# Kernel tuning notes

Hardware: AMD Instinct MI355X
Metric: run time of the kernel (lower is better)

## Reference

```python
import jax, jax.numpy as jnp
from jax import lax
import numpy as np

B, N, K, H = 8, 4096, 24, 32  # graphs, nodes/graph, kNN k, hidden_dim


def setup_inputs() -> dict:
    key = jax.random.key(0)
    ks = jax.random.split(key, 16)
    W = lambda k, i, o: jax.random.normal(k, (i, o), jnp.float32) * 0.1
    b = lambda k, o: jax.random.normal(k, (o,), jnp.float32) * 0.01
    inp = {
        'x_lc': jax.random.normal(ks[0], (B * N, 4), jnp.float32),
        'batch_lc': jnp.repeat(jnp.arange(B, dtype=jnp.int64), N),
        'enc_w1': W(ks[1], 4, H), 'enc_b1': b(ks[2], H),
        'enc_w2': W(ks[3], H, H), 'enc_b2': b(ks[4], H),
        'conv1_w': W(ks[5], 2 * H, H), 'conv1_b': b(ks[6], H),
        'conv2_w': W(ks[7], 2 * H, H), 'conv2_b': b(ks[8], H),
        'conv3_w': W(ks[9], 2 * H, H), 'conv3_b': b(ks[10], H),
        'out_w1': W(ks[11], H, 32), 'out_b1': b(ks[12], 32),
        'out_w2': W(ks[13], 32, 16), 'out_b2': b(ks[14], 16),
        'out_w3': W(ks[15], 16, 8), 'out_b3': jnp.zeros((8,), jnp.float32),
    }
    return inp


def _dynamic_edge_conv(x, w, bias):
    # x: [B, N, D]; kNN within each graph, edge msg nn([x_i, x_j - x_i]), max-agg
    d2 = jnp.sum(x * x, axis=-1)  # [B, N]
    dist = d2[:, :, None] + d2[:, None, :] - 2.0 * jnp.einsum('bnd,bmd->bnm', x, x)
    # kNN index computation is non-differentiable (as in PyG knn)
    idx = lax.top_k(-lax.stop_gradient(dist), K)[1]  # [B, N, K], includes self
    xj = jax.vmap(lambda xb, ib: xb[ib])(x, idx)  # [B, N, K, D]
    xi = jnp.broadcast_to(x[:, :, None, :], xj.shape)
    e = jnp.concatenate([xi, xj - xi], axis=-1)  # [B, N, K, 2D]
    h = jax.nn.elu(e @ w + bias)  # [B, N, K, H]
    return jnp.max(h, axis=2)  # [B, N, H]


def reference(x_lc, batch_lc, enc_w1, enc_b1, enc_w2, enc_b2,
              conv1_w, conv1_b, conv2_w, conv2_b, conv3_w, conv3_b,
              out_w1, out_b1, out_w2, out_b2, out_w3, out_b3):
    # lc_encode
    h = jax.nn.elu(x_lc @ enc_w1 + enc_b1)
    h = jax.nn.elu(h @ enc_w2 + enc_b2)  # [B*N, H]
    h = h.reshape(B, N, H)  # equal-sized sorted graphs
    h = _dynamic_edge_conv(h, conv1_w, conv1_b)
    h = _dynamic_edge_conv(h, conv2_w, conv2_b)
    h = _dynamic_edge_conv(h, conv3_w, conv3_b)
    h = h.reshape(B * N, H)
    o = jax.nn.elu(h @ out_w1 + out_b1)
    o = jax.nn.elu(o @ out_w2 + out_b2)
    o = o @ out_w3 + out_b3  # [B*N, 8]
    return (o, batch_lc)
```

## Files before the change

kernel.cpp:

```cpp
#include <hip/hip_runtime.h>
#include <cstddef>
#include <cstdint>

#define BN    32768
#define NG    4096
#define KNN   24
#define KPW   14
#define KM    32
#define CHK   128
#define NBQ   64
#define STKD  16
#define TRIG  13

typedef float f32x4_t __attribute__((ext_vector_type(4)));
typedef short s16x8_t __attribute__((ext_vector_type(8)));

__device__ __forceinline__ float elu_f(float x) {
    return x > 0.f ? x : expm1f(x);
}

__device__ __forceinline__ unsigned short f2bf(float f) {
    unsigned u = __float_as_uint(f);
    unsigned r = (u + 0x7FFFu + ((u >> 16) & 1u)) >> 16;
    return (unsigned short)r;
}

__device__ __forceinline__ void gload_lds16(const void* g, void* l) {
    __builtin_amdgcn_global_load_lds(
        (const __attribute__((address_space(1))) unsigned*)g,
        (__attribute__((address_space(3))) unsigned*)l, 16, 0, 0);
}

__device__ __forceinline__ void pack_node(int n, const float* hv,
    unsigned short* __restrict__ hbf, unsigned short* __restrict__ til,
    float* __restrict__ d2b)
{
    __align__(16) unsigned short us[32];
    float s = 0.f;
#pragma unroll
    for (int k = 0; k < 32; ++k) {
        us[k] = f2bf(hv[k]);
        float v = __uint_as_float(((unsigned)us[k]) << 16);
        s = fmaf(v, v, s);
    }
    d2b[n] = s;
    const uint4* up = reinterpret_cast<const uint4*>(us);
    uint4* lp = reinterpret_cast<uint4*>(hbf + (size_t)n * 32);
#pragma unroll
    for (int j = 0; j < 4; ++j) lp[j] = up[j];
    const int g = n >> 12, ln = n & 4095, tile = ln >> 4, c = ln & 15;
    unsigned short* tb = til + (size_t)g * 131072 + tile * 512 + c * 8;
#pragma unroll
    for (int kg = 0; kg < 4; ++kg)
        *reinterpret_cast<uint4*>(tb + kg * 128) = up[kg];
}

__global__ __launch_bounds__(128) void k_encoder(
    const float* __restrict__ x,
    const float* __restrict__ w1, const float* __restrict__ b1,
    const float* __restrict__ w2, const float* __restrict__ b2,
    float* __restrict__ hOut, float* __restrict__ d2Out,
    unsigned short* __restrict__ hbf, unsigned short* __restrict__ til,
    float* __restrict__ d2b)
{
    __shared__ float sw1[4 * 32];
    __shared__ float sb1[32];
    __shared__ float sw2[32 * 32];
    __shared__ float sb2[32];
    int tid = threadIdx.x;
    sw1[tid] = w1[tid];
    if (tid < 32) sb1[tid] = b1[tid];
    for (int i = tid; i < 1024; i += 128) sw2[i] = w2[i];
    if (tid >= 32 && tid < 64) sb2[tid - 32] = b2[tid - 32];
    __syncthreads();

    int node = blockIdx.x * 128 + tid;
    float4 xv = reinterpret_cast<const float4*>(x)[node];

    float h1[32];
#pragma unroll
    for (int o = 0; o < 32; ++o) {
        float s = sb1[o];
        s = fmaf(xv.x, sw1[o], s);
        s = fmaf(xv.y, sw1[32 + o], s);
        s = fmaf(xv.z, sw1[64 + o], s);
        s = fmaf(xv.w, sw1[96 + o], s);
        h1[o] = elu_f(s);
    }
    float h2[32];
    float d2 = 0.f;
#pragma unroll
    for (int o = 0; o < 32; ++o) {
        float s = sb2[o];
#pragma unroll
        for (int f = 0; f < 32; ++f) s = fmaf(h1[f], sw2[f * 32 + o], s);
        float v = elu_f(s);
        h2[o] = v;
        d2 = fmaf(v, v, d2);
    }
    float4* hp = reinterpret_cast<float4*>(hOut) + (size_t)node * 8;
#pragma unroll
    for (int j = 0; j < 8; ++j)
        hp[j] = make_float4(h2[4 * j], h2[4 * j + 1], h2[4 * j + 2], h2[4 * j + 3]);
    d2Out[node] = d2;
    pack_node(node, h2, hbf, til, d2b);
}

#define CHAIN14(nk_) do { \
    unsigned nk = (nk_); \
    _Pragma("unroll") \
    for (int jj = 0; jj < KPW; ++jj) { \
        unsigned tj = top[jj]; \
        unsigned lo = nk < tj ? nk : tj; \
        unsigned hi = nk < tj ? tj : nk; \
        top[jj] = lo; nk = hi; \
    } \
} while (0)

__global__ __launch_bounds__(512, 4) void k_scan(
    const unsigned short* __restrict__ til,
    const unsigned short* __restrict__ hbf,
    const float* __restrict__ d2b,
    unsigned short* __restrict__ mgs)
{
    __shared__ __align__(16) unsigned char smem[49152];
    constexpr int SD2 = 0;
    constexpr int STK = 16384;
    constexpr int LST = 16384;

    const int tid = threadIdx.x;
    const int lane = tid & 63;
    const int wid = __builtin_amdgcn_readfirstlane(tid >> 6);
    const int qt = wid >> 1;
    const int par = wid & 1;
    const int bid = blockIdx.x;
    const int g = bid >> 6;
    const int gbase = g << 12;
    const int blockq = (bid & 63) * NBQ;
    const int qnode = gbase + blockq + qt * 16 + (lane & 15);
    const int rg = (lane >> 4) * 4;

    gload_lds16(d2b + gbase + wid * 256 + lane * 4, smem + SD2 + wid * 1024);
    gload_lds16(d2b + gbase + 2048 + wid * 256 + lane * 4,
                smem + SD2 + 8192 + wid * 1024);

    s16x8_t bfrag = *reinterpret_cast<const s16x8_t*>(
        hbf + (size_t)qnode * 32 + (lane >> 4) * 8);
    const float qd2 = d2b[qnode];
    const float nqd2h = -0.5f * qd2;

    unsigned top[KPW];
#pragma unroll
    for (int j = 0; j < KPW; ++j) top[j] = 0xFFFFFFFFu;
    unsigned thresh = 0xFFFFFFFFu;
    int pcnt = 0;

    const char* gtw = (const char*)til + (size_t)g * 262144
                    + (size_t)par * 1024 + (size_t)lane * 16;
    const float* d2s = reinterpret_cast<const float*>(smem + SD2);
    unsigned* stkl = reinterpret_cast<unsigned*>(smem + STK + wid * 4096) + lane;

    __syncthreads();

    s16x8_t af[4];
#pragma unroll
    for (int i = 0; i < 4; ++i)
        af[i] = *reinterpret_cast<const s16x8_t*>(gtw + i * 2048);

    for (int c = 0; c < 32; ++c) {
        s16x8_t an[4];
        if (c < 31) {
#pragma unroll
            for (int i = 0; i < 4; ++i)
                an[i] = *reinterpret_cast<const s16x8_t*>(
                    gtw + (size_t)(c + 1) * 8192 + i * 2048);
        } else {
#pragma unroll
            for (int i = 0; i < 4; ++i) an[i] = af[i];
        }
        f32x4_t cv[4];
#pragma unroll
        for (int i = 0; i < 4; ++i)
            cv[i] = *reinterpret_cast<const f32x4_t*>(
                d2s + c * 128 + (i * 2 + par) * 16 + rg);
#pragma unroll
        for (int i = 0; i < 4; ++i) {
            const int t = i * 2 + par;
            f32x4_t acc;
#pragma unroll
            for (int r = 0; r < 4; ++r) acc[r] = fmaf(-0.5f, cv[i][r], nqd2h);
            acc = __builtin_amdgcn_mfma_f32_16x16x32_bf16(af[i], bfrag, acc, 0, 0, 0);
            const int cid0 = c * CHK + t * 16 + rg;
#pragma unroll
            for (int r = 0; r < 4; ++r) {
                unsigned key = (__float_as_uint(acc[r]) & 0xFFFFF000u)
                             | (unsigned)(cid0 + r);
                stkl[pcnt * 64] = key;
                pcnt += (key < thresh) ? 1 : 0;
            }
            if (__any(pcnt >= TRIG)) {
#pragma unroll 1
                for (int j = 0; j < STKD; ++j) {
                    if (!__any(pcnt > j)) break;
                    unsigned kk = stkl[j * 64];
                    unsigned k = (j < pcnt) ? kk : 0xFFFFFFFFu;
                    CHAIN14(k);
                }
                pcnt = 0;
                thresh = top[KPW - 1];
            }
        }
#pragma unroll
        for (int i = 0; i < 4; ++i) af[i] = an[i];
    }
#pragma unroll 1
    for (int j = 0; j < STKD; ++j) {
        if (!__any(pcnt > j)) break;
        unsigned kk = stkl[j * 64];
        unsigned k = (j < pcnt) ? kk : 0xFFFFFFFFu;
        CHAIN14(k);
    }
    __syncthreads();

    unsigned* lst = reinterpret_cast<unsigned*>(smem + LST);
    const int q_d  = qt * 16 + (lane & 15);
    const int li_d = par * 4 + (lane >> 4);
    {
        unsigned* myrow = lst + q_d * 120 + li_d * 15;
#pragma unroll
        for (int j = 0; j < KPW; ++j) myrow[j] = top[j];
    }
    __syncthreads();

    {
        int rk[KPW];
#pragma unroll
        for (int j = 0; j < KPW; ++j) rk[j] = j;
        const unsigned* base = lst + q_d * 120;
#pragma unroll 1
        for (int u = 1; u < 8; ++u) {
            const unsigned* pl = base + ((li_d + u) & 7) * 15;
            unsigned pk[KPW];
#pragma unroll
            for (int k = 0; k < KPW; ++k) pk[k] = pl[k];
#pragma unroll
            for (int k = 0; k < KPW; ++k) {
#pragma unroll
                for (int j = 0; j < KPW; ++j)
                    rk[j] += (pk[k] < top[j]) ? 1 : 0;
            }
        }
        unsigned short* mrow = mgs + (size_t)(gbase + blockq + q_d) * 32;
#pragma unroll
        for (int j = 0; j < KPW; ++j)
            if (rk[j] < KM) mrow[rk[j]] = (unsigned short)(top[j] & 0xFFFu);
    }
}

__global__ __launch_bounds__(128) void k_refine(
    const unsigned short* __restrict__ mgs,
    const float* __restrict__ hf,
    const float* __restrict__ d2x,
    const float* __restrict__ cw, const float* __restrict__ cb,
    int* __restrict__ idxOut,
    float* __restrict__ Abuf, float* __restrict__ Bbuf)
{
    __shared__ float sw[2048];
    __shared__ float sb[32];

    const int tid = threadIdx.x;
    const int bid = blockIdx.x;
    const int g = bid >> 8;
    const int gbase = g << 12;
    const int blockq = (bid & 255) * 16;

    for (int i = tid; i < 2048; i += 128) sw[i] = cw[i];
    if (tid < 32) sb[tid] = cb[tid];
    __syncthreads();

    const int q  = tid >> 3;
    const int s0 = tid & 7;
    const int qn = gbase + blockq + q;

    const float4* qp = reinterpret_cast<const float4*>(hf) + (size_t)qn * 8;
    float4 qf[8];
#pragma unroll
    for (int j = 0; j < 8; ++j) qf[j] = qp[j];
    const float qd2e = d2x[qn];

    int cids[4];
    float d[4];
#pragma unroll
    for (int ss = 0; ss < 4; ++ss) {
        const int s = s0 + ss * 8;
        const int cid = (int)mgs[(size_t)qn * 32 + s];
        cids[ss] = cid;
        const int cn = gbase + cid;
        const float4* cp = reinterpret_cast<const float4*>(hf) + (size_t)cn * 8;
        float ax = 0.f, ay = 0.f, az = 0.f, aw = 0.f;
#pragma unroll
        for (int jj = 0; jj < 8; ++jj) {
            float4 cc = cp[jj];
            ax = fmaf(qf[jj].x, cc.x, ax);
            ay = fmaf(qf[jj].y, cc.y, ay);
            az = fmaf(qf[jj].z, cc.z, az);
            aw = fmaf(qf[jj].w, cc.w, aw);
        }
        float dot = (ax + ay) + (az + aw);
        d[ss] = fmaf(-2.f, dot, qd2e + d2x[cn]);
    }

    {
        int rk[4];
#pragma unroll
        for (int i = 0; i < 4; ++i) {
            int r = 0;
#pragma unroll
            for (int j = 0; j < 4; ++j) {
                if (j != i)
                    r += (d[j] < d[i] || (d[j] == d[i] && j < i)) ? 1 : 0;
            }
            rk[i] = r;
        }
#pragma unroll
        for (int t = 1; t < 8; ++t) {
            float pd[4];
#pragma unroll
            for (int ss = 0; ss < 4; ++ss) pd[ss] = __shfl_xor(d[ss], t);
            const int ps0 = s0 ^ t;
#pragma unroll
            for (int i = 0; i < 4; ++i) {
                const int mys = s0 + 8 * i;
#pragma unroll
                for (int ss = 0; ss < 4; ++ss) {
                    const int pss = ps0 + 8 * ss;
                    rk[i] += (pd[ss] < d[i] ||
                              (pd[ss] == d[i] && pss < mys)) ? 1 : 0;
                }
            }
        }
        int* o = idxOut + (size_t)qn * KNN;
#pragma unroll
        for (int i = 0; i < 4; ++i)
            if (rk[i] < KNN) o[rk[i]] = cids[i];
    }

    {
        const int o0 = s0 * 4;
        float hreg[32];
#pragma unroll
        for (int j = 0; j < 8; ++j) {
            hreg[4 * j]     = qf[j].x; hreg[4 * j + 1] = qf[j].y;
            hreg[4 * j + 2] = qf[j].z; hreg[4 * j + 3] = qf[j].w;
        }
        float4 s1 = make_float4(0.f, 0.f, 0.f, 0.f);
        float4 s2 = make_float4(0.f, 0.f, 0.f, 0.f);
#pragma unroll
        for (int f = 0; f < 32; ++f) {
            float hv = hreg[f];
            float4 wa = *reinterpret_cast<const float4*>(sw + f * 32 + o0);
            float4 wb = *reinterpret_cast<const float4*>(sw + (32 + f) * 32 + o0);
            s1.x = fmaf(hv, wa.x, s1.x); s1.y = fmaf(hv, wa.y, s1.y);
            s1.z = fmaf(hv, wa.z, s1.z); s1.w = fmaf(hv, wa.w, s1.w);
            s2.x = fmaf(hv, wb.x, s2.x); s2.y = fmaf(hv, wb.y, s2.y);
            s2.z = fmaf(hv, wb.z, s2.z); s2.w = fmaf(hv, wb.w, s2.w);
        }
        float4 bv = *reinterpret_cast<const float4*>(sb + o0);
        float4 av = make_float4(s1.x - s2.x + bv.x, s1.y - s2.y + bv.y,
                                s1.z - s2.z + bv.z, s1.w - s2.w + bv.w);
        *reinterpret_cast<float4*>(Abuf + (size_t)qn * 32 + o0) = av;
        *reinterpret_cast<float4*>(Bbuf + (size_t)qn * 32 + o0) = s2;
    }
}

template <bool LAST>
__global__ __launch_bounds__(128) void k_aggregate(
    const float* __restrict__ A, const float* __restrict__ Bv,
    const int* __restrict__ idx,
    float* __restrict__ hOut, float* __restrict__ d2Out,
    unsigned short* __restrict__ hbf, unsigned short* __restrict__ til,
    float* __restrict__ d2b,
    const float* __restrict__ w1, const float* __restrict__ b1,
    const float* __restrict__ w2, const float* __restrict__ b2,
    const float* __restrict__ w3, const float* __restrict__ b3,
    float* __restrict__ out)
{
    __shared__ float sw1[1024];
    __shared__ float sb1[32];
    __shared__ float sw2[512];
    __shared__ float sb2[16];
    __shared__ float sw3[128];
    __shared__ float sb3[8];
    int tid = threadIdx.x;
    if (LAST) {
        for (int i = tid; i < 1024; i += 128) sw1[i] = w1[i];
        for (int i = tid; i < 512; i += 128) sw2[i] = w2[i];
        sw3[tid] = w3[tid];
        if (tid < 32) sb1[tid] = b1[tid];
        if (tid >= 32 && tid < 48) sb2[tid - 32] = b2[tid - 32];
        if (tid >= 48 && tid < 56) sb3[tid - 48] = b3[tid - 48];
        __syncthreads();
    }

    int node = blockIdx.x * 128 + tid;
    int g = node >> 12;
    const int* ip = idx + (size_t)node * KNN;

    float4 m[8];
#pragma unroll
    for (int j = 0; j < 8; ++j) m[j] = make_float4(-1e30f, -1e30f, -1e30f, -1e30f);

    for (int k = 0; k < KNN; ++k) {
        int cand = (g << 12) + ip[k];
        const float4* bp = reinterpret_cast<const float4*>(Bv) + (size_t)cand * 8;
#pragma unroll
        for (int j = 0; j < 8; ++j) {
            float4 b = bp[j];
            m[j].x = fmaxf(m[j].x, b.x);
            m[j].y = fmaxf(m[j].y, b.y);
            m[j].z = fmaxf(m[j].z, b.z);
            m[j].w = fmaxf(m[j].w, b.w);
        }
    }
    const float4* ap = reinterpret_cast<const float4*>(A) + (size_t)node * 8;
    float hv[32];
    float d2 = 0.f;
#pragma unroll
    for (int j = 0; j < 8; ++j) {
        float4 a = ap[j];
        float4 v;
        v.x = elu_f(a.x + m[j].x);
        v.y = elu_f(a.y + m[j].y);
        v.z = elu_f(a.z + m[j].z);
        v.w = elu_f(a.w + m[j].w);
        d2 = fmaf(v.x, v.x, d2);
        d2 = fmaf(v.y, v.y, d2);
        d2 = fmaf(v.z, v.z, d2);
        d2 = fmaf(v.w, v.w, d2);
        hv[4 * j] = v.x; hv[4 * j + 1] = v.y; hv[4 * j + 2] = v.z; hv[4 * j + 3] = v.w;
    }

    if (!LAST) {
        float4* hp = reinterpret_cast<float4*>(hOut) + (size_t)node * 8;
#pragma unroll
        for (int j = 0; j < 8; ++j)
            hp[j] = make_float4(hv[4 * j], hv[4 * j + 1], hv[4 * j + 2], hv[4 * j + 3]);
        d2Out[node] = d2;
        pack_node(node, hv, hbf, til, d2b);
    } else {
        float o1[32];
#pragma unroll
        for (int o = 0; o < 32; ++o) {
            float s = sb1[o];
#pragma unroll
            for (int f = 0; f < 32; ++f) s = fmaf(hv[f], sw1[f * 32 + o], s);
            o1[o] = elu_f(s);
        }
        float o2[16];
#pragma unroll
        for (int o = 0; o < 16; ++o) {
            float s = sb2[o];
#pragma unroll
            for (int f = 0; f < 32; ++f) s = fmaf(o1[f], sw2[f * 16 + o], s);
            o2[o] = elu_f(s);
        }
        float o3[8];
#pragma unroll
        for (int o = 0; o < 8; ++o) {
            float s = sb3[o];
#pragma unroll
            for (int f = 0; f < 16; ++f) s = fmaf(o2[f], sw3[f * 8 + o], s);
            o3[o] = s;
        }
        float4* op = reinterpret_cast<float4*>(out) + (size_t)node * 2;
        op[0] = make_float4(o3[0], o3[1], o3[2], o3[3]);
        op[1] = make_float4(o3[4], o3[5], o3[6], o3[7]);
        out[(size_t)BN * 8 + node] = (float)(node >> 12);
    }
}

extern "C" void kernel_launch(void* const* d_in, const int* in_sizes, int n_in,
                              void* d_out, int out_size, void* d_ws, size_t ws_size,
                              hipStream_t stream)
{
    (void)in_sizes; (void)n_in; (void)out_size; (void)ws_size;
    const float* x      = (const float*)d_in[0];
    const float* enc_w1 = (const float*)d_in[2];
    const float* enc_b1 = (const float*)d_in[3];
    const float* enc_w2 = (const float*)d_in[4];
    const float* enc_b2 = (const float*)d_in[5];
    const float* conv_w[3] = { (const float*)d_in[6], (const float*)d_in[8], (const float*)d_in[10] };
    const float* conv_b[3] = { (const float*)d_in[7], (const float*)d_in[9], (const float*)d_in[11] };
    const float* out_w1 = (const float*)d_in[12];
    const float* out_b1 = (const float*)d_in[13];
    const float* out_w2 = (const float*)d_in[14];
    const float* out_b2 = (const float*)d_in[15];
    const float* out_w3 = (const float*)d_in[16];
    const float* out_b3 = (const float*)d_in[17];

    char* ws = (char*)d_ws;
    float*          hA   = (float*)(ws + 0);
    float*          hB   = (float*)(ws + 4194304);
    unsigned short* hbfA = (unsigned short*)(ws + 8388608);
    unsigned short* hbfB = (unsigned short*)(ws + 10485760);
    unsigned short* tilA = (unsigned short*)(ws + 12582912);
    unsigned short* tilB = (unsigned short*)(ws + 14680064);
    float*          d2A  = (float*)(ws + 16777216);
    float*          d2B  = (float*)(ws + 16908288);
    float*          d2bA = (float*)(ws + 17039360);
    float*          d2bB = (float*)(ws + 17170432);
    int*            idx  = (int*)(ws + 17301504);
    float*          Abuf = (float*)(ws + 20447232);
    float*          Bbuf = (float*)(ws + 24641536);

    k_encoder<<<256, 128, 0, stream>>>(x, enc_w1, enc_b1, enc_w2, enc_b2,
                                       hA, d2A, hbfA, tilA, d2bA);

    float* hin = hA;   float* d2in = d2A;   float* d2bin = d2bA;
    unsigned short* hbfin = hbfA; unsigned short* tilin = tilA;
    float* hout = hB;  float* d2out = d2B;  float* d2bout = d2bB;
    unsigned short* hbfout = hbfB; unsigned short* tilout = tilB;

    for (int l = 0; l < 3; ++l) {
        unsigned short* mgs = tilout;
        k_scan<<<512, 512, 0, stream>>>(tilin, hbfin, d2bin, mgs);
        k_refine<<<2048, 128, 0, stream>>>(mgs, hin, d2in,
                                           conv_w[l], conv_b[l], idx, Abuf, Bbuf);
        if (l < 2) {
            k_aggregate<false><<<256, 128, 0, stream>>>(
                Abuf, Bbuf, idx, hout, d2out, hbfout, tilout, d2bout,
                nullptr, nullptr, nullptr, nullptr, nullptr, nullptr, nullptr);
        } else {
            k_aggregate<true><<<256, 128, 0, stream>>>(
                Abuf, Bbuf, idx, nullptr, nullptr, nullptr, nullptr, nullptr,
                out_w1, out_b1, out_w2, out_b2, out_w3, out_b3, (float*)d_out);
        }
        float* tf; unsigned short* ts;
        tf = hin; hin = hout; hout = tf;
        tf = d2in; d2in = d2out; d2out = tf;
        tf = d2bin; d2bin = d2bout; d2bout = tf;
        ts = hbfin; hbfin = hbfout; hbfout = ts;
        ts = tilin; tilin = tilout; tilout = ts;
    }
}
```

Measured before the change: 528.9 us.

## Split candidate distance dot products across 8 lanes with shuffle reduction in refine

```diff
diff --git a/kernel.cpp b/kernel.cpp
--- a/kernel.cpp
+++ b/kernel.cpp
@@ -267,6 +267,7 @@
 {
     __shared__ float sw[2048];
     __shared__ float sb[32];
+    __shared__ __align__(16) float shq[16][32];
 
     const int tid = threadIdx.x;
     const int bid = blockIdx.x;
@@ -274,90 +275,65 @@
     const int gbase = g << 12;
     const int blockq = (bid & 255) * 16;
 
-    for (int i = tid; i < 2048; i += 128) sw[i] = cw[i];
-    if (tid < 32) sb[tid] = cb[tid];
-    __syncthreads();
-
     const int q  = tid >> 3;
     const int s0 = tid & 7;
     const int qn = gbase + blockq + q;
 
-    const float4* qp = reinterpret_cast<const float4*>(hf) + (size_t)qn * 8;
-    float4 qf[8];
-#pragma unroll
-    for (int j = 0; j < 8; ++j) qf[j] = qp[j];
+    const float4 qc = reinterpret_cast<const float4*>(hf)[(size_t)qn * 8 + s0];
+
+    for (int i = tid; i < 2048; i += 128) sw[i] = cw[i];
+    if (tid < 32) sb[tid] = cb[tid];
+    *reinterpret_cast<float4*>(&shq[q][s0 * 4]) = qc;
+    __syncthreads();
+
     const float qd2e = d2x[qn];
 
-    int cids[4];
-    float d[4];
-#pragma unroll
-    for (int ss = 0; ss < 4; ++ss) {
-        const int s = s0 + ss * 8;
+    float dall[32];
+    float d_own[4];
+    int cid_own[4];
+#pragma unroll
+    for (int i = 0; i < 4; ++i) { d_own[i] = 0.f; cid_own[i] = 0; }
+#pragma unroll
+    for (int s = 0; s < 32; ++s) {
         const int cid = (int)mgs[(size_t)qn * 32 + s];
-        cids[ss] = cid;
         const int cn = gbase + cid;
-        const float4* cp = reinterpret_cast<const float4*>(hf) + (size_t)cn * 8;
-        float ax = 0.f, ay = 0.f, az = 0.f, aw = 0.f;
-#pragma unroll
-        for (int jj = 0; jj < 8; ++jj) {
-            float4 cc = cp[jj];
-            ax = fmaf(qf[jj].x, cc.x, ax);
-            ay = fmaf(qf[jj].y, cc.y, ay);
-            az = fmaf(qf[jj].z, cc.z, az);
-            aw = fmaf(qf[jj].w, cc.w, aw);
-        }
-        float dot = (ax + ay) + (az + aw);
-        d[ss] = fmaf(-2.f, dot, qd2e + d2x[cn]);
+        const float4 cc = reinterpret_cast<const float4*>(hf)[(size_t)cn * 8 + s0];
+        float p = qc.x * cc.x;
+        p = fmaf(qc.y, cc.y, p);
+        p = fmaf(qc.z, cc.z, p);
+        p = fmaf(qc.w, cc.w, p);
+        p += __shfl_xor(p, 1, 8);
+        p += __shfl_xor(p, 2, 8);
+        p += __shfl_xor(p, 4, 8);
+        const float dv = fmaf(-2.f, p, qd2e + d2x[cn]);
+        dall[s] = dv;
+        const bool own = ((s & 7) == s0);
+        d_own[s >> 3]   = own ? dv  : d_own[s >> 3];
+        cid_own[s >> 3] = own ? cid : cid_own[s >> 3];
     }
 
     {
-        int rk[4];
+        int* o = idxOut + (size_t)qn * KNN;
 #pragma unroll
         for (int i = 0; i < 4; ++i) {
-            int r = 0;
-#pragma unroll
-            for (int j = 0; j < 4; ++j) {
-                if (j != i)
-                    r += (d[j] < d[i] || (d[j] == d[i] && j < i)) ? 1 : 0;
-            }
-            rk[i] = r;
-        }
-#pragma unroll
-        for (int t = 1; t < 8; ++t) {
-            float pd[4];
-#pragma unroll
-            for (int ss = 0; ss < 4; ++ss) pd[ss] = __shfl_xor(d[ss], t);
-            const int ps0 = s0 ^ t;
-#pragma unroll
-            for (int i = 0; i < 4; ++i) {
-                const int mys = s0 + 8 * i;
-#pragma unroll
-                for (int ss = 0; ss < 4; ++ss) {
-                    const int pss = ps0 + 8 * ss;
-                    rk[i] += (pd[ss] < d[i] ||
-                              (pd[ss] == d[i] && pss < mys)) ? 1 : 0;
-                }
-            }
-        }
-        int* o = idxOut + (size_t)qn * KNN;
-#pragma unroll
-        for (int i = 0; i < 4; ++i)
-            if (rk[i] < KNN) o[rk[i]] = cids[i];
+            const int mys = s0 + 8 * i;
+            const float di = d_own[i];
+            int rank = 0;
+#pragma unroll
+            for (int j = 0; j < 32; ++j)
+                rank += (dall[j] < di || (dall[j] == di && j < mys)) ? 1 : 0;
+            if (rank < KNN) o[rank] = cid_own[i];
+        }
     }
 
     {
         const int o0 = s0 * 4;
-        float hreg[32];
-#pragma unroll
-        for (int j = 0; j < 8; ++j) {
-            hreg[4 * j]     = qf[j].x; hreg[4 * j + 1] = qf[j].y;
-            hreg[4 * j + 2] = qf[j].z; hreg[4 * j + 3] = qf[j].w;
-        }
+        const float* hr = shq[q];
         float4 s1 = make_float4(0.f, 0.f, 0.f, 0.f);
         float4 s2 = make_float4(0.f, 0.f, 0.f, 0.f);
 #pragma unroll
         for (int f = 0; f < 32; ++f) {
-            float hv = hreg[f];
+            float hv = hr[f];
             float4 wa = *reinterpret_cast<const float4*>(sw + f * 32 + o0);
             float4 wb = *reinterpret_cast<const float4*>(sw + (32 + f) * 32 + o0);
             s1.x = fmaf(hv, wa.x, s1.x); s1.y = fmaf(hv, wa.y, s1.y);
```

Result: faster. 502.1 us (median of 2 runs) (-5.1%).
